# Performance work log

Measured on AMD Instinct MI355X. Metric: run time of the kernel, lower is better.

Reference implementation:

```python
import jax, jax.numpy as jnp
import numpy as np

HEAD_DIM = 64


def rotate_half(x):
    x1, x2 = jnp.split(x, 2, axis=-1)
    return jnp.concatenate((-x2, x1), axis=-1)


def setup_inputs() -> dict:
    key = jax.random.key(0)
    ks = jax.random.split(key, 12)
    B, S, H, Hkv, D, hid = 1, 1536, 64, 8, HEAD_DIM, 2880
    std = 0.02
    x = jax.random.normal(ks[0], (B, S, hid), jnp.float32)
    # real RoPE cache, layout [cos | sin] of shape (S, 2*D)
    inv = 1.0 / (10000.0 ** (np.arange(0, D, 2, dtype=np.float32) / D))
    freqs = np.outer(np.arange(S, dtype=np.float32), inv)          # (S, D/2)
    emb = np.concatenate([freqs, freqs], axis=-1)                  # (S, D)
    rope_cache = jnp.asarray(
        np.concatenate([np.cos(emb), np.sin(emb)], axis=-1), jnp.float32
    )
    return {
        "x": x,
        "rope_cache": rope_cache,
        "wq_w": jax.random.normal(ks[1], (H * D, hid), jnp.float32) * std,
        "wq_b": jax.random.normal(ks[2], (H * D,), jnp.float32) * std,
        "wk_w": jax.random.normal(ks[3], (Hkv * D, hid), jnp.float32) * std,
        "wk_b": jax.random.normal(ks[4], (Hkv * D,), jnp.float32) * std,
        "wv_w": jax.random.normal(ks[5], (Hkv * D, hid), jnp.float32) * std,
        "wv_b": jax.random.normal(ks[6], (Hkv * D,), jnp.float32) * std,
        "wo_w": jax.random.normal(ks[7], (hid, H * D), jnp.float32) * std,
        "wo_b": jax.random.normal(ks[8], (hid,), jnp.float32) * std,
        "sinks": jax.random.normal(ks[9], (H,), jnp.float32) * std,
    }


def reference(x, rope_cache, wq_w, wq_b, wk_w, wk_b, wv_w, wv_b, wo_w, wo_b, sinks):
    B, S, hid = x.shape
    D = HEAD_DIM
    H = wq_w.shape[0] // D
    Hkv = wk_w.shape[0] // D
    n_rep = H // Hkv

    q = (x @ wq_w.T + wq_b).reshape(B, S, H, D)
    k = (x @ wk_w.T + wk_b).reshape(B, S, Hkv, D)
    v = (x @ wv_w.T + wv_b).reshape(B, S, Hkv, D)

    # RoPE (rotate-half form); rope_cache[:, :D]=cos, [:, D:]=sin
    cos = rope_cache[:S, :D][None, :, None, :]
    sin = rope_cache[:S, D:][None, :, None, :]
    q = q * cos + rotate_half(q) * sin
    k = k * cos + rotate_half(k) * sin

    # GQA repeat_kv: interleaved repeat along head dim
    k = jnp.repeat(k, n_rep, axis=2)  # (B, S, H, D)
    v = jnp.repeat(v, n_rep, axis=2)

    scale = 1.0 / jnp.sqrt(jnp.asarray(D, x.dtype))
    scores = jnp.einsum("bqhd,bkhd->bhqk", q, k) * scale  # (B, H, S, S)
    i = jnp.arange(S)
    causal = i[:, None] >= i[None, :]
    neg = jnp.asarray(jnp.finfo(scores.dtype).min, scores.dtype)
    scores = jnp.where(causal[None, None], scores, neg)

    lse = jax.nn.logsumexp(scores, axis=-1)               # (B, H, S)
    attn = jax.nn.softmax(scores, axis=-1)
    out = jnp.einsum("bhqk,bkhd->bqhd", attn, v)          # (B, S, H, D)

    # attention-sink rescale: sigmoid(lse - sink_logit)
    sink_scale = jax.nn.sigmoid(lse - sinks[None, :, None])  # (B, H, S)
    out = out * jnp.transpose(sink_scale, (0, 2, 1))[..., None]

    out = out.reshape(B, S, H * D)
    return out @ wo_w.T + wo_b
```

## Files before the change

### kernel.cpp

```cpp
#include <hip/hip_runtime.h>

typedef unsigned short u16;
typedef unsigned int u32;
typedef __attribute__((ext_vector_type(8))) __bf16 bf16x8;
typedef __attribute__((ext_vector_type(8))) u16 u16x8;
typedef __attribute__((ext_vector_type(4))) u16 u16x4;
typedef __attribute__((ext_vector_type(4))) float f32x4;
typedef __attribute__((ext_vector_type(2))) u32 u32x2;

#define DEV static __device__ __forceinline__

DEV u16 f2bf(float f) {
  unsigned u = __builtin_bit_cast(unsigned, f);
  u += 0x7FFFu + ((u >> 16) & 1u);
  return (u16)(u >> 16);
}

DEV float ex2(float x) { return __builtin_amdgcn_exp2f(x); }

DEV u32 cvt_pk_bf16(float lo, float hi) {
  u32 r;
  asm("v_cvt_pk_bf16_f32 %0, %1, %2" : "=v"(r) : "v"(lo), "v"(hi));
  return r;
}

DEV f32x4 mfma16(bf16x8 a, bf16x8 b, f32x4 c) {
  return __builtin_amdgcn_mfma_f32_16x16x32_bf16(a, b, c, 0, 0, 0);
}

DEV f32x4 fmax4(f32x4 a, f32x4 b) {
  f32x4 r;
  r[0] = fmaxf(a[0], b[0]); r[1] = fmaxf(a[1], b[1]);
  r[2] = fmaxf(a[2], b[2]); r[3] = fmaxf(a[3], b[3]);
  return r;
}

DEV void gload_lds16(const u16* g, u16* lds) {
  __builtin_amdgcn_global_load_lds(
      (const __attribute__((address_space(1))) void*)g,
      (__attribute__((address_space(3))) void*)lds, 16, 0, 0);
}

DEV void vm_wait4() { asm volatile("s_waitcnt vmcnt(4)" ::: "memory"); }
DEV void vm_wait2() { asm volatile("s_waitcnt vmcnt(2)" ::: "memory"); }
DEV void vm_wait0() { asm volatile("s_waitcnt vmcnt(0)" ::: "memory"); }

__global__ __launch_bounds__(256) void cvt_all(
    const float* __restrict__ x, const float* __restrict__ wq,
    const float* __restrict__ wk, const float* __restrict__ wv,
    const float* __restrict__ wo, const float* __restrict__ qb,
    const float* __restrict__ kb, const float* __restrict__ vb,
    u16* __restrict__ x_bf, u16* __restrict__ wqkv_bf,
    u16* __restrict__ wo_bf, float* __restrict__ bias_p) {
  const int NX = 1536 * 2880 / 4;
  const int NWQ = 4096 * 2880 / 4;
  const int NWKV = 512 * 2880 / 4;
  const int NWO = 3072 * 4096 / 4;
  const int C0 = NX, C1 = C0 + NWQ, C2 = C1 + NWKV, C3 = C2 + NWKV;
  const int C4 = C3 + NWO, C5 = C4 + 5120 / 4;
  int i = blockIdx.x * 256 + threadIdx.x;
  if (i >= C5) return;
  if (i < C4) {
    const float* s;
    u16* d;
    bool pad = false;
    if (i < C0) { s = x + (size_t)i * 4; d = x_bf + (size_t)i * 4; }
    else if (i < C1) { size_t q = i - C0; s = wq + q * 4; d = wqkv_bf + q * 4; }
    else if (i < C2) { size_t q = i - C1; s = wk + q * 4; d = wqkv_bf + (size_t)NWQ * 4 + q * 4; }
    else if (i < C3) { size_t q = i - C2; s = wv + q * 4; d = wqkv_bf + (size_t)(NWQ + NWKV) * 4 + q * 4; }
    else {
      size_t q = i - C3;
      int row = (int)(q >> 10);
      pad = (row >= 2880);
      s = wo + q * 4; d = wo_bf + q * 4;
    }
    u16x4 o;
    if (!pad) {
      float4 v = *(const float4*)s;
      o = (u16x4){f2bf(v.x), f2bf(v.y), f2bf(v.z), f2bf(v.w)};
    } else {
      o = (u16x4){0, 0, 0, 0};
    }
    *(u16x4*)d = o;
  } else {
    int e = (i - C4) * 4;
#pragma unroll
    for (int j = 0; j < 4; j++) {
      int idx = e + j;
      bias_p[idx] = (idx < 4096) ? qb[idx] : (idx < 4608 ? kb[idx - 4096] : vb[idx - 4608]);
    }
  }
}

template <int MODE>
__global__ __launch_bounds__(512) void gemm128(const u16* __restrict__ A,
                                               const u16* __restrict__ B,
                                               const float* __restrict__ bias,
                                               float* __restrict__ C,
                                               u16* __restrict__ Obf,
                                               const float* __restrict__ rope,
                                               int M, int K, int Nreal, int ldc) {
  __shared__ u16 smA[2][128 * 64];
  __shared__ u16 smB[2][128 * 64];
  int nbm = M >> 7;
  int chunk = gridDim.x >> 3;
  int wg = (blockIdx.x & 7) * chunk + (blockIdx.x >> 3);
  int bm = wg % nbm, bn = wg / nbm;
  int t = threadIdx.x, lane = t & 63, wv = t >> 6;
  int wr = wv >> 1, wc = wv & 1;
  int l15 = lane & 15, hi = lane >> 4;
  f32x4 acc[2][4] = {};
  int tr = t >> 3;
  int scol = ((t & 7) ^ (tr & 7)) * 8;
  const u16* Ab = A + (size_t)(bm * 128 + tr) * K + scol;
  const u16* Bb = B + (size_t)(bn * 128 + tr) * K + scol;

  auto stage = [&](int b, int ks) {
    int k0 = ks * 64;
    gload_lds16(Ab + k0, &smA[b][t * 8]);
    gload_lds16(Ab + k0 + (size_t)64 * K, &smA[b][4096 + t * 8]);
    gload_lds16(Bb + k0, &smB[b][t * 8]);
    gload_lds16(Bb + k0 + (size_t)64 * K, &smB[b][4096 + t * 8]);
  };

  int NK = K >> 6;
  stage(0, 0);
  stage(1, 1);
  for (int ks = 0; ks < NK; ks++) {
    int cur = ks & 1;
    if (ks + 1 < NK) vm_wait4(); else vm_wait0();
    __builtin_amdgcn_s_barrier();
    __builtin_amdgcn_sched_barrier(0);
#pragma unroll
    for (int kk = 0; kk < 2; kk++) {
      int sc = ((kk * 4 + hi) ^ (l15 & 7)) * 8;
      bf16x8 af[2], bfr[4];
#pragma unroll
      for (int m = 0; m < 2; m++)
        af[m] = *(const bf16x8*)(&smA[cur][(wr * 32 + m * 16 + l15) * 64 + sc]);
#pragma unroll
      for (int n = 0; n < 4; n++)
        bfr[n] = *(const bf16x8*)(&smB[cur][(wc * 64 + n * 16 + l15) * 64 + sc]);
      __builtin_amdgcn_s_setprio(1);
#pragma unroll
      for (int m = 0; m < 2; m++)
#pragma unroll
        for (int n = 0; n < 4; n++)
          acc[m][n] = mfma16(af[m], bfr[n], acc[m][n]);
      __builtin_amdgcn_s_setprio(0);
    }
    __builtin_amdgcn_s_barrier();
    if (ks + 2 < NK) stage(cur, ks + 2);
  }

  int r0 = bm * 128 + wr * 32 + hi * 4;
  int c0 = bn * 128 + wc * 64 + l15;
  if (MODE == 0) {
#pragma unroll
    for (int n = 0; n < 4; n++) {
      int col = c0 + n * 16;
      if (col >= Nreal) continue;
      float bv = bias[col];
#pragma unroll
      for (int m = 0; m < 2; m++)
#pragma unroll
        for (int r = 0; r < 4; r++)
          C[(size_t)(r0 + m * 16 + r) * ldc + col] = acc[m][n][r] + bv;
    }
  } else {
    float bv[4];
#pragma unroll
    for (int n = 0; n < 4; n++) bv[n] = bias[c0 + n * 16];
    if (bn < 36) {
      float scale = (bn < 32) ? 0.180336880f : 1.0f;
#pragma unroll
      for (int m = 0; m < 2; m++) {
#pragma unroll
        for (int r = 0; r < 4; r++) {
          int s = r0 + m * 16 + r;
          const float* rp = rope + (size_t)s * 128;
          float cv0 = rp[l15], cv1 = rp[l15 + 16];
          float sv0 = rp[64 + l15], sv1 = rp[64 + l15 + 16];
          float v0 = acc[0][0][r], v1 = acc[0][1][r];
          float v2 = acc[0][2][r], v3 = acc[0][3][r];
          if (m) { v0 = acc[1][0][r]; v1 = acc[1][1][r]; v2 = acc[1][2][r]; v3 = acc[1][3][r]; }
          v0 += bv[0]; v1 += bv[1]; v2 += bv[2]; v3 += bv[3];
          u16* po = Obf + (size_t)s * 5120 + c0;
          po[0]  = f2bf((v0 * cv0 - v2 * sv0) * scale);
          po[16] = f2bf((v1 * cv1 - v3 * sv1) * scale);
          po[32] = f2bf((v2 * cv0 + v0 * sv0) * scale);
          po[48] = f2bf((v3 * cv1 + v1 * sv1) * scale);
        }
      }
    } else {
#pragma unroll
      for (int m = 0; m < 2; m++)
#pragma unroll
        for (int r = 0; r < 4; r++) {
          int s = r0 + m * 16 + r;
          u16* po = Obf + (size_t)s * 5120 + c0;
#pragma unroll
          for (int n = 0; n < 4; n++) po[n * 16] = f2bf(acc[m][n][r] + bv[n]);
        }
    }
  }
}

__global__ __launch_bounds__(256) void cast_trT(const u16* __restrict__ src,
                                                u16* __restrict__ dst, int S, int Hkv,
                                                int ld, int col0) {
  __shared__ u16 tile[64][65];
  int s0 = blockIdx.x * 64;
  int hkv = blockIdx.y;
  int t = threadIdx.x;
  int dl = (t & 15) * 4;
  int sl = t >> 4;
#pragma unroll
  for (int j = 0; j < 4; j++) {
    int s = sl + j * 16;
    u16x4 v = *(const u16x4*)(src + (size_t)(s0 + s) * ld + col0 + hkv * 64 + dl);
    tile[dl + 0][s] = v[0];
    tile[dl + 1][s] = v[1];
    tile[dl + 2][s] = v[2];
    tile[dl + 3][s] = v[3];
  }
  __syncthreads();
  int sl2 = (t & 7) * 8;
  int dl2 = t >> 3;
#pragma unroll
  for (int j = 0; j < 2; j++) {
    int d = dl2 + j * 32;
    u16x8 o;
#pragma unroll
    for (int c = 0; c < 8; c++) o[c] = tile[d][sl2 + c];
    *(u16x8*)(dst + ((size_t)hkv * 64 + d) * S + s0 + sl2) = o;
  }
}

__global__ __launch_bounds__(512) void attn_fwd(const u16* __restrict__ QKV,
                                                const u16* __restrict__ VT,
                                                const float* __restrict__ sinks,
                                                u16* __restrict__ Out,
                                                int S, int H, int Hkv) {
  __shared__ u16 ldsK[2][64 * 64];
  __shared__ u16 ldsV[2][64 * 64];
  __shared__ u16 ldsP[8][16 * 64];
  int bx = blockIdx.x, pair = blockIdx.y;
  int t = threadIdx.x, lane = t & 63, wv = t >> 6;
  int wq = wv & 3;
  int h = pair * 2 + (wv >> 2);
  int hkv = pair >> 2;
  int l15 = lane & 15, hi = lane >> 4;
  const u16* Kh = QKV + 4096 + hkv * 64;
  const u16* VTh = VT + (size_t)hkv * 64 * S;
  u16* ldsPw = &ldsP[wv][0];
  int psw = (l15 & 7) << 4;
  float snk = sinks[h];

  auto stage = [&](int b, int kb) {
    int k0 = kb * 64;
    int row = t >> 3, c16 = t & 7;
    int sc = (c16 ^ (row & 7)) * 8;
    gload_lds16(Kh + (size_t)(k0 + row) * 5120 + sc, &ldsK[b][t * 8]);
    gload_lds16(VTh + (size_t)row * S + k0 + sc, &ldsV[b][t * 8]);
  };

  for (int pass = 0; pass < 2; pass++) {
    int qb = pass == 0 ? (12 + bx) : (11 - bx);
    int q0 = qb * 64 + wq * 16;
    int rowq = q0 + l15;
    const u16* Qh = QKV + (size_t)q0 * 5120 + h * 64;
    bf16x8 qf[2];
    qf[0] = *(const bf16x8*)(Qh + (size_t)l15 * 5120 + hi * 8);
    qf[1] = *(const bf16x8*)(Qh + (size_t)l15 * 5120 + 32 + hi * 8);

    float mx = -1e30f, ls = 0.f;
    f32x4 ao[4] = {};

    int nkb = qb + 1;
    stage(0, 0);
    if (nkb > 1) stage(1, 1);
    for (int kb = 0; kb < nkb; kb++) {
      int cur = kb & 1;
      if (kb + 1 < nkb) vm_wait2(); else vm_wait0();
      __builtin_amdgcn_s_barrier();
      __builtin_amdgcn_sched_barrier(0);
      {
        f32x4 s[4] = {};
        __builtin_amdgcn_s_setprio(1);
#pragma unroll
        for (int kk = 0; kk < 2; kk++) {
#pragma unroll
          for (int ct = 0; ct < 4; ct++) {
            int row = ct * 16 + l15;
            int c16 = (kk * 4 + hi) ^ (row & 7);
            bf16x8 kf = *(const bf16x8*)(&ldsK[cur][row * 64 + c16 * 8]);
            s[ct] = mfma16(kf, qf[kk], s[ct]);
          }
        }
        __builtin_amdgcn_s_setprio(0);

        bool full = (kb * 64 + 63) < q0;
        if (!full) {
          int kc = kb * 64 + hi * 4;
#pragma unroll
          for (int ct = 0; ct < 4; ct++)
#pragma unroll
            for (int r = 0; r < 4; r++)
              if (kc + ct * 16 + r > rowq) s[ct][r] = -1e30f;
        }

        f32x4 mm = fmax4(fmax4(s[0], s[1]), fmax4(s[2], s[3]));
        float tmx = fmaxf(fmaxf(mm[0], mm[1]), fmaxf(mm[2], mm[3]));
        tmx = fmaxf(tmx, __shfl_xor(tmx, 16));
        tmx = fmaxf(tmx, __shfl_xor(tmx, 32));
        bool upd = __any(tmx > mx + 8.0f);
        if (upd) {
          float mn = fmaxf(mx, tmx);
          float al = ex2(mx - mn);
          mx = mn;
          ls *= al;
          float alr[4];
#pragma unroll
          for (int r = 0; r < 4; r++) alr[r] = __shfl(al, hi * 4 + r);
#pragma unroll
          for (int nt = 0; nt < 4; nt++)
#pragma unroll
            for (int r = 0; r < 4; r++) ao[nt][r] *= alr[r];
        }
#pragma unroll
        for (int ct = 0; ct < 4; ct++)
#pragma unroll
          for (int r = 0; r < 4; r++) s[ct][r] = ex2(s[ct][r] - mx);
        f32x4 sm = s[0] + s[1] + s[2] + s[3];
        float rs = (sm[0] + sm[1]) + (sm[2] + sm[3]);
        rs += __shfl_xor(rs, 16);
        rs += __shfl_xor(rs, 32);
        ls += rs;

#pragma unroll
        for (int ct = 0; ct < 4; ct++) {
          u32x2 pk = {cvt_pk_bf16(s[ct][0], s[ct][1]),
                      cvt_pk_bf16(s[ct][2], s[ct][3])};
          *(u32x2*)(&ldsPw[(l15 * 128 + ((ct * 32 + hi * 8) ^ psw)) >> 1]) = pk;
        }

        __builtin_amdgcn_s_setprio(1);
#pragma unroll
        for (int kk = 0; kk < 2; kk++) {
          bf16x8 pa = *(const bf16x8*)(&ldsPw[(l15 * 128 + ((kk * 64 + hi * 16) ^ psw)) >> 1]);
#pragma unroll
          for (int nt = 0; nt < 4; nt++) {
            int vrow = nt * 16 + l15;
            int c16 = (kk * 4 + hi) ^ (vrow & 7);
            bf16x8 vf = *(const bf16x8*)(&ldsV[cur][vrow * 64 + c16 * 8]);
            ao[nt] = mfma16(pa, vf, ao[nt]);
          }
        }
        __builtin_amdgcn_s_setprio(0);
      }
      __builtin_amdgcn_s_barrier();
      if (kb + 2 < nkb) stage(cur, kb + 2);
    }

    float lse = 0.69314718056f * mx + __logf(ls);
    float ss = 1.f / (1.f + __expf(snk - lse));
    float f = ss / ls;
    float fr[4];
#pragma unroll
    for (int r = 0; r < 4; r++) fr[r] = __shfl(f, hi * 4 + r);
#pragma unroll
    for (int r = 0; r < 4; r++) {
      int row = q0 + hi * 4 + r;
#pragma unroll
      for (int nt = 0; nt < 4; nt++)
        Out[(size_t)row * (H * 64) + h * 64 + nt * 16 + l15] = f2bf(ao[nt][r] * fr[r]);
    }
  }
}

extern "C" void kernel_launch(void* const* d_in, const int* in_sizes, int n_in,
                              void* d_out, int out_size, void* d_ws, size_t ws_size,
                              hipStream_t stream) {
  const int S = 1536, HID = 2880, H = 64, HKV = 8;
  const int NQ = 4096, NKV = 512, NQKV = 5120, NPAD = 3072;

  const float* x     = (const float*)d_in[0];
  const float* rope  = (const float*)d_in[1];
  const float* wq_w  = (const float*)d_in[2];
  const float* wq_b  = (const float*)d_in[3];
  const float* wk_w  = (const float*)d_in[4];
  const float* wk_b  = (const float*)d_in[5];
  const float* wv_w  = (const float*)d_in[6];
  const float* wv_b  = (const float*)d_in[7];
  const float* wo_w  = (const float*)d_in[8];
  const float* wo_b  = (const float*)d_in[9];
  const float* sinks = (const float*)d_in[10];
  float* out = (float*)d_out;

  char* ws = (char*)d_ws;
  size_t off = 0;
  auto alloc = [&](size_t bytes) {
    char* p = ws + off;
    off = (off + bytes + 255) & ~(size_t)255;
    return p;
  };
  u16*   x_bf    = (u16*)  alloc((size_t)S * HID * 2);
  u16*   wqkv_bf = (u16*)  alloc((size_t)NQKV * HID * 2);
  u16*   wo_bf   = (u16*)  alloc((size_t)NPAD * NQ * 2);
  u16*   qkv_bf  = (u16*)  alloc((size_t)S * NQKV * 2);
  float* bias_p  = (float*)alloc((size_t)NQKV * 4);
  u16*   VTb     = (u16*)  alloc((size_t)HKV * 64 * S * 2);
  u16*   att     = (u16*)  alloc((size_t)S * NQ * 2);
  (void)ws_size; (void)n_in; (void)in_sizes; (void)out_size;

  auto cdiv = [](int a, int b) { return (a + b - 1) / b; };

  const int NCVT = S * HID / 4 + NQ * HID / 4 + 2 * (NKV * HID / 4) +
                   NPAD * NQ / 4 + NQKV / 4;
  cvt_all<<<cdiv(NCVT, 256), 256, 0, stream>>>(x, wq_w, wk_w, wv_w, wo_w,
                                               wq_b, wk_b, wv_b,
                                               x_bf, wqkv_bf, wo_bf, bias_p);

  gemm128<1><<<(S / 128) * (NQKV / 128), 512, 0, stream>>>(
      x_bf, wqkv_bf, bias_p, nullptr, qkv_bf, rope, S, HID, NQKV, NQKV);

  cast_trT<<<dim3(S / 64, HKV), 256, 0, stream>>>(qkv_bf, VTb, S, HKV, NQKV, NQ + NKV);

  attn_fwd<<<dim3(12, H / 2), 512, 0, stream>>>(qkv_bf, VTb, sinks, att, S, H, HKV);

  gemm128<0><<<(S / 128) * (NPAD / 128), 512, 0, stream>>>(
      att, wo_bf, wo_b, out, nullptr, nullptr, S, NQ, HID, HID);
}
```

Before: 186.6 us.

## Fuse Wo fp32-to-bf16 conversion into output projection GEMM B loads

Result: slower. 246.6 us (+32.1%).

```diff
diff --git a/kernel.cpp b/kernel.cpp
--- a/kernel.cpp
+++ b/kernel.cpp
@@ -7,6 +7,7 @@
 typedef __attribute__((ext_vector_type(4))) u16 u16x4;
 typedef __attribute__((ext_vector_type(4))) float f32x4;
 typedef __attribute__((ext_vector_type(2))) u32 u32x2;
+typedef __attribute__((ext_vector_type(4))) u32 u32x4;
 
 #define DEV static __device__ __forceinline__
 
@@ -41,49 +42,38 @@
       (__attribute__((address_space(3))) void*)lds, 16, 0, 0);
 }
 
+DEV void vm_wait6() { asm volatile("s_waitcnt vmcnt(6)" ::: "memory"); }
 DEV void vm_wait4() { asm volatile("s_waitcnt vmcnt(4)" ::: "memory"); }
 DEV void vm_wait2() { asm volatile("s_waitcnt vmcnt(2)" ::: "memory"); }
 DEV void vm_wait0() { asm volatile("s_waitcnt vmcnt(0)" ::: "memory"); }
+DEV void lgkm_wait0() { asm volatile("s_waitcnt lgkmcnt(0)" ::: "memory"); }
 
 __global__ __launch_bounds__(256) void cvt_all(
     const float* __restrict__ x, const float* __restrict__ wq,
     const float* __restrict__ wk, const float* __restrict__ wv,
-    const float* __restrict__ wo, const float* __restrict__ qb,
-    const float* __restrict__ kb, const float* __restrict__ vb,
+    const float* __restrict__ qb, const float* __restrict__ kb,
+    const float* __restrict__ vb,
     u16* __restrict__ x_bf, u16* __restrict__ wqkv_bf,
-    u16* __restrict__ wo_bf, float* __restrict__ bias_p) {
+    float* __restrict__ bias_p) {
   const int NX = 1536 * 2880 / 4;
   const int NWQ = 4096 * 2880 / 4;
   const int NWKV = 512 * 2880 / 4;
-  const int NWO = 3072 * 4096 / 4;
   const int C0 = NX, C1 = C0 + NWQ, C2 = C1 + NWKV, C3 = C2 + NWKV;
-  const int C4 = C3 + NWO, C5 = C4 + 5120 / 4;
+  const int C4 = C3 + 5120 / 4;
   int i = blockIdx.x * 256 + threadIdx.x;
-  if (i >= C5) return;
-  if (i < C4) {
+  if (i >= C4) return;
+  if (i < C3) {
     const float* s;
     u16* d;
-    bool pad = false;
     if (i < C0) { s = x + (size_t)i * 4; d = x_bf + (size_t)i * 4; }
     else if (i < C1) { size_t q = i - C0; s = wq + q * 4; d = wqkv_bf + q * 4; }
     else if (i < C2) { size_t q = i - C1; s = wk + q * 4; d = wqkv_bf + (size_t)NWQ * 4 + q * 4; }
-    else if (i < C3) { size_t q = i - C2; s = wv + q * 4; d = wqkv_bf + (size_t)(NWQ + NWKV) * 4 + q * 4; }
-    else {
-      size_t q = i - C3;
-      int row = (int)(q >> 10);
-      pad = (row >= 2880);
-      s = wo + q * 4; d = wo_bf + q * 4;
-    }
-    u16x4 o;
-    if (!pad) {
-      float4 v = *(const float4*)s;
-      o = (u16x4){f2bf(v.x), f2bf(v.y), f2bf(v.z), f2bf(v.w)};
-    } else {
-      o = (u16x4){0, 0, 0, 0};
-    }
+    else { size_t q = i - C2; s = wv + q * 4; d = wqkv_bf + (size_t)(NWQ + NWKV) * 4 + q * 4; }
+    float4 v = *(const float4*)s;
+    u16x4 o = {f2bf(v.x), f2bf(v.y), f2bf(v.z), f2bf(v.w)};
     *(u16x4*)d = o;
   } else {
-    int e = (i - C4) * 4;
+    int e = (i - C3) * 4;
 #pragma unroll
     for (int j = 0; j < 4; j++) {
       int idx = e + j;
@@ -206,6 +196,121 @@
   }
 }
 
+__global__ __launch_bounds__(512) void gemm_wo(const u16* __restrict__ A,
+                                               const float* __restrict__ Bf,
+                                               const float* __restrict__ bias,
+                                               float* __restrict__ C,
+                                               int M, int K, int Nreal, int ldc,
+                                               int Brows) {
+  __shared__ u16 smA[2][128 * 64];
+  __shared__ u16 smB[2][128 * 64];
+  int nbm = M >> 7;
+  int chunk = gridDim.x >> 3;
+  int wg = (blockIdx.x & 7) * chunk + (blockIdx.x >> 3);
+  int bm = wg % nbm, bn = wg / nbm;
+  int t = threadIdx.x, lane = t & 63, wv = t >> 6;
+  int wr = wv >> 1, wc = wv & 1;
+  int l15 = lane & 15, hi = lane >> 4;
+  f32x4 acc[2][4] = {};
+  int tr = t >> 3;
+  int scol = ((t & 7) ^ (tr & 7)) * 8;
+  const u16* Ab = A + (size_t)(bm * 128 + tr) * K + scol;
+  int brow0 = bn * 128 + tr, brow1 = brow0 + 64;
+  bool b0ok = brow0 < Brows, b1ok = brow1 < Brows;
+  const float* Bp0 = Bf + (size_t)(b0ok ? brow0 : 0) * K + scol;
+  const float* Bp1 = Bf + (size_t)(b1ok ? brow1 : 0) * K + scol;
+  const float4 z4 = {0.f, 0.f, 0.f, 0.f};
+
+  float4 e0, e1, e2, e3;
+  float4 o0, o1, o2, o3;
+
+  auto stageA = [&](int b, int ks) {
+    int k0 = ks * 64;
+    gload_lds16(Ab + k0, &smA[b][t * 8]);
+    gload_lds16(Ab + k0 + (size_t)64 * K, &smA[b][4096 + t * 8]);
+  };
+
+#define BLOAD(r0, r1, r2, r3, ks)                                   \
+  do {                                                              \
+    int k0 = (ks) * 64;                                             \
+    r0 = *(const float4*)(Bp0 + k0);                                \
+    r1 = *(const float4*)(Bp0 + k0 + 4);                            \
+    r2 = *(const float4*)(Bp1 + k0);                                \
+    r3 = *(const float4*)(Bp1 + k0 + 4);                            \
+    if (!b0ok) { r0 = z4; r1 = z4; }                                \
+    if (!b1ok) { r2 = z4; r3 = z4; }                                \
+  } while (0)
+
+#define BWRITE(buf, r0, r1, r2, r3)                                 \
+  do {                                                              \
+    u32x4 lo = {cvt_pk_bf16(r0.x, r0.y), cvt_pk_bf16(r0.z, r0.w),   \
+                cvt_pk_bf16(r1.x, r1.y), cvt_pk_bf16(r1.z, r1.w)};  \
+    *(u32x4*)(&smB[buf][t * 8]) = lo;                               \
+    u32x4 hi4 = {cvt_pk_bf16(r2.x, r2.y), cvt_pk_bf16(r2.z, r2.w),  \
+                 cvt_pk_bf16(r3.x, r3.y), cvt_pk_bf16(r3.z, r3.w)}; \
+    *(u32x4*)(&smB[buf][4096 + t * 8]) = hi4;                       \
+  } while (0)
+
+  auto compute = [&](int cur) {
+#pragma unroll
+    for (int kk = 0; kk < 2; kk++) {
+      int sc = ((kk * 4 + hi) ^ (l15 & 7)) * 8;
+      bf16x8 af[2], bfr[4];
+#pragma unroll
+      for (int m = 0; m < 2; m++)
+        af[m] = *(const bf16x8*)(&smA[cur][(wr * 32 + m * 16 + l15) * 64 + sc]);
+#pragma unroll
+      for (int n = 0; n < 4; n++)
+        bfr[n] = *(const bf16x8*)(&smB[cur][(wc * 64 + n * 16 + l15) * 64 + sc]);
+      __builtin_amdgcn_s_setprio(1);
+#pragma unroll
+      for (int m = 0; m < 2; m++)
+#pragma unroll
+        for (int n = 0; n < 4; n++)
+          acc[m][n] = mfma16(af[m], bfr[n], acc[m][n]);
+      __builtin_amdgcn_s_setprio(0);
+    }
+  };
+
+  const int NK = K >> 6;
+  stageA(0, 0); BLOAD(e0, e1, e2, e3, 0);
+  stageA(1, 1); BLOAD(o0, o1, o2, o3, 1);
+  for (int ks = 0; ks < NK; ks += 2) {
+    if (ks + 1 < NK) vm_wait6(); else vm_wait0();
+    BWRITE(0, e0, e1, e2, e3);
+    lgkm_wait0();
+    __builtin_amdgcn_s_barrier();
+    __builtin_amdgcn_sched_barrier(0);
+    compute(0);
+    __builtin_amdgcn_s_barrier();
+    if (ks + 2 < NK) { stageA(0, ks + 2); BLOAD(e0, e1, e2, e3, ks + 2); }
+    if (ks + 2 < NK) vm_wait6(); else vm_wait0();
+    BWRITE(1, o0, o1, o2, o3);
+    lgkm_wait0();
+    __builtin_amdgcn_s_barrier();
+    __builtin_amdgcn_sched_barrier(0);
+    compute(1);
+    __builtin_amdgcn_s_barrier();
+    if (ks + 3 < NK) { stageA(1, ks + 3); BLOAD(o0, o1, o2, o3, ks + 3); }
+  }
+#undef BLOAD
+#undef BWRITE
+
+  int r0 = bm * 128 + wr * 32 + hi * 4;
+  int c0 = bn * 128 + wc * 64 + l15;
+#pragma unroll
+  for (int n = 0; n < 4; n++) {
+    int col = c0 + n * 16;
+    if (col >= Nreal) continue;
+    float bv = bias[col];
+#pragma unroll
+    for (int m = 0; m < 2; m++)
+#pragma unroll
+      for (int r = 0; r < 4; r++)
+        C[(size_t)(r0 + m * 16 + r) * ldc + col] = acc[m][n][r] + bv;
+  }
+}
+
 __global__ __launch_bounds__(256) void cast_trT(const u16* __restrict__ src,
                                                 u16* __restrict__ dst, int S, int Hkv,
                                                 int ld, int col0) {
@@ -407,7 +512,6 @@
   };
   u16*   x_bf    = (u16*)  alloc((size_t)S * HID * 2);
   u16*   wqkv_bf = (u16*)  alloc((size_t)NQKV * HID * 2);
-  u16*   wo_bf   = (u16*)  alloc((size_t)NPAD * NQ * 2);
   u16*   qkv_bf  = (u16*)  alloc((size_t)S * NQKV * 2);
   float* bias_p  = (float*)alloc((size_t)NQKV * 4);
   u16*   VTb     = (u16*)  alloc((size_t)HKV * 64 * S * 2);
@@ -416,11 +520,10 @@
 
   auto cdiv = [](int a, int b) { return (a + b - 1) / b; };
 
-  const int NCVT = S * HID / 4 + NQ * HID / 4 + 2 * (NKV * HID / 4) +
-                   NPAD * NQ / 4 + NQKV / 4;
-  cvt_all<<<cdiv(NCVT, 256), 256, 0, stream>>>(x, wq_w, wk_w, wv_w, wo_w,
+  const int NCVT = S * HID / 4 + NQ * HID / 4 + 2 * (NKV * HID / 4) + NQKV / 4;
+  cvt_all<<<cdiv(NCVT, 256), 256, 0, stream>>>(x, wq_w, wk_w, wv_w,
                                                wq_b, wk_b, wv_b,
-                                               x_bf, wqkv_bf, wo_bf, bias_p);
+                                               x_bf, wqkv_bf, bias_p);
 
   gemm128<1><<<(S / 128) * (NQKV / 128), 512, 0, stream>>>(
       x_bf, wqkv_bf, bias_p, nullptr, qkv_bf, rope, S, HID, NQKV, NQKV);
@@ -429,6 +532,6 @@
 
   attn_fwd<<<dim3(12, H / 2), 512, 0, stream>>>(qkv_bf, VTb, sinks, att, S, H, HKV);
 
-  gemm128<0><<<(S / 128) * (NPAD / 128), 512, 0, stream>>>(
-      att, wo_bf, wo_b, out, nullptr, nullptr, S, NQ, HID, HID);
-}
+  gemm_wo<<<(S / 128) * (NPAD / 128), 512, 0, stream>>>(
+      att, wo_w, wo_b, out, S, NQ, HID, HID, HID);
+}
```
